# Kernel optimization log

Hardware: AMD Instinct MI355X
Metric: run time of the kernel (lower is better)

Reference implementation:

```python
import jax, jax.numpy as jnp
import numpy as np

B, S, D = 16, 1024, 1024
H, HD = 16, 64  # head_dim = D // H
INIT_STD = 0.002
DEFAULT_BETA = 1.0 / np.sqrt(HD)


def setup_inputs() -> dict:
    key = jax.random.key(0)
    k1, k2, k3 = jax.random.split(key, 3)
    x = jax.random.normal(k1, (B, S, D), dtype=jnp.float32)
    q_proj_weight = jax.random.normal(k2, (H, HD, D), dtype=jnp.float32) * INIT_STD
    k_proj_weight = jax.random.normal(k3, (H, HD, D), dtype=jnp.float32) * INIT_STD
    beta = jnp.full((H,), DEFAULT_BETA, dtype=jnp.float32)
    return {"x": x, "q_proj_weight": q_proj_weight, "k_proj_weight": k_proj_weight, "beta": beta}


def reference(x, q_proj_weight, k_proj_weight, beta):
    # q, k: (B, S, H, HD)
    q = jnp.einsum('bse,hde->bshd', x, q_proj_weight)
    k = jnp.einsum('bse,hde->bshd', x, k_proj_weight)
    # scores: (B, H, S_query, S_key) with per-head beta temperature
    scores = jnp.einsum('bshd,bthd,h->bhst', q, k, beta)
    # self-attention exclusion: mask the diagonal (B == C) with -inf
    seq = scores.shape[-1]
    diag = jnp.eye(seq, dtype=bool)
    scores = jnp.where(diag[None, None], -jnp.inf, scores)
    # stable logsumexp over keys, then energy = -sum_h,s lse / beta_h
    lse = jax.nn.logsumexp(scores, axis=-1)  # (B, H, S)
    energy = -(lse / beta[None, :, None]).sum()
    return energy
```

## Files before the change

### kernel.cpp

```cpp
#include <hip/hip_runtime.h>
#include <hip/hip_bf16.h>


using short8  = __attribute__((ext_vector_type(8))) short;
using f32x4   = __attribute__((ext_vector_type(4))) float;
using ushort8 = __attribute__((ext_vector_type(8))) unsigned short;
using float4v = __attribute__((ext_vector_type(4))) float;

#define B_  16
#define S_  1024
#define D_  1024
#define H_  16
#define HD_ 64

__device__ inline unsigned short f2bf(float f) {
  union { float f; unsigned u; } v; v.f = f;
  unsigned r = v.u + 0x7FFFu + ((v.u >> 16) & 1u);
  return (unsigned short)(r >> 16);
}

__global__ __launch_bounds__(256) void cvt_bf16_k(const float* __restrict__ in,
                                                  unsigned short* __restrict__ out, int n8) {
  int i = blockIdx.x * 256 + threadIdx.x;
  if (i >= n8) return;
  const float4v* p = (const float4v*)in;
  float4v a = p[2 * i], b = p[2 * i + 1];
  ushort8 r;
  r[0] = f2bf(a[0]); r[1] = f2bf(a[1]); r[2] = f2bf(a[2]); r[3] = f2bf(a[3]);
  r[4] = f2bf(b[0]); r[5] = f2bf(b[1]); r[6] = f2bf(b[2]); r[7] = f2bf(b[3]);
  ((ushort8*)out)[i] = r;
}

__global__ void zero_out_k(float* o) { if (threadIdx.x == 0) *o = 0.f; }

__device__ inline void gload_lds16(const void* g, void* l) {
  __builtin_amdgcn_global_load_lds((const __attribute__((address_space(1))) void*)g,
                                   (__attribute__((address_space(3))) void*)l, 16, 0, 0);
}

__device__ inline void stage_tile(const char* src, int stride, char* lds, int tid) {
  int lane = tid & 63, wave = tid >> 6;
#pragma unroll
  for (int r = 0; r < 4; ++r) {
    int o   = r * 4096 + wave * 1024 + lane * 16;
    int row = o >> 7;
    int kb  = o & 127;
    int skb = kb ^ ((row & 7) << 4);
    gload_lds16(src + (size_t)row * stride + skb, lds + (r * 4096 + wave * 1024));
  }
}

__device__ inline short8 ld_frag(const char* lds, int row, int kk, int lane) {
  int kb   = kk * 64 + ((lane >> 4) << 4);
  int addr = row * 128 + (kb ^ ((row & 7) << 4));
  return *(const short8*)(lds + addr);
}

__global__ __launch_bounds__(256) void proj_gemm_k(const unsigned short* __restrict__ Xb,
                                                   const unsigned short* __restrict__ Wqb,
                                                   const unsigned short* __restrict__ Wkb,
                                                   unsigned short* __restrict__ Qg,
                                                   unsigned short* __restrict__ Kg) {
  __shared__ char As[16384];
  __shared__ char Bs[16384];
  const int tid = threadIdx.x, lane = tid & 63, wave = tid >> 6;
  const int wr = wave >> 1, wc = wave & 1;
  const int m0 = blockIdx.x * 128, n0 = blockIdx.y * 128;
  const unsigned short* W = blockIdx.z ? Wkb : Wqb;
  unsigned short* Out = blockIdx.z ? Kg : Qg;
  const char* Abase = (const char*)Xb + (size_t)m0 * (D_ * 2);
  const char* Bbase = (const char*)W  + (size_t)n0 * (D_ * 2);

  f32x4 acc[4][4];
#pragma unroll
  for (int i = 0; i < 4; ++i)
#pragma unroll
    for (int j = 0; j < 4; ++j)
#pragma unroll
      for (int q = 0; q < 4; ++q) acc[i][j][q] = 0.f;

  for (int kt = 0; kt < D_ / 64; ++kt) {
    stage_tile(Abase + kt * 128, D_ * 2, As, tid);
    stage_tile(Bbase + kt * 128, D_ * 2, Bs, tid);
    __syncthreads();
#pragma unroll
    for (int kk = 0; kk < 2; ++kk) {
      short8 a[4], b[4];
#pragma unroll
      for (int i = 0; i < 4; ++i) a[i] = ld_frag(As, wr * 64 + i * 16 + (lane & 15), kk, lane);
#pragma unroll
      for (int i = 0; i < 4; ++i) b[i] = ld_frag(Bs, wc * 64 + i * 16 + (lane & 15), kk, lane);
#pragma unroll
      for (int i = 0; i < 4; ++i)
#pragma unroll
        for (int j = 0; j < 4; ++j)
          acc[i][j] = __builtin_amdgcn_mfma_f32_16x16x32_bf16(a[i], b[j], acc[i][j], 0, 0, 0);
    }
    __syncthreads();
  }

#pragma unroll
  for (int mi = 0; mi < 4; ++mi)
#pragma unroll
    for (int ni = 0; ni < 4; ++ni)
#pragma unroll
      for (int j = 0; j < 4; ++j) {
        int m = m0 + wr * 64 + mi * 16 + ((lane >> 4) << 2) + j;
        int n = n0 + wc * 64 + ni * 16 + (lane & 15);
        int bb = m >> 10, s = m & (S_ - 1);
        int h = n >> 6, hd = n & (HD_ - 1);
        Out[(((size_t)bb * H_ + h) * S_ + s) * HD_ + hd] = f2bf(acc[mi][ni][j]);
      }
}

__global__ __launch_bounds__(256) void attn_lse_k(const unsigned short* __restrict__ Qg,
                                                  const unsigned short* __restrict__ Kg,
                                                  const float* __restrict__ beta,
                                                  float* __restrict__ out) {
  __shared__ char Qs[16384];
  __shared__ char Ks[16384];
  __shared__ float wsum[4];
  const int tid = threadIdx.x, lane = tid & 63, wave = tid >> 6;
  const int qt = blockIdx.x, h = blockIdx.y, b = blockIdx.z;
  const int q0 = qt * 128;
  const char* qbase = (const char*)Qg + (((size_t)b * H_ + h) * S_) * (HD_ * 2);
  const char* kbase = (const char*)Kg + (((size_t)b * H_ + h) * S_) * (HD_ * 2);

  stage_tile(qbase + (size_t)q0 * 128, 128, Qs, tid);
  const float bet = beta[h];

  float l_run[2][4];
#pragma unroll
  for (int mi = 0; mi < 2; ++mi)
#pragma unroll
    for (int j = 0; j < 4; ++j) l_run[mi][j] = 0.f;

  for (int kt = 0; kt < 8; ++kt) {
    stage_tile(kbase + (size_t)kt * 128 * 128, 128, Ks, tid);
    __syncthreads();

    f32x4 acc[2][8];
#pragma unroll
    for (int i = 0; i < 2; ++i)
#pragma unroll
      for (int j = 0; j < 8; ++j)
#pragma unroll
        for (int q = 0; q < 4; ++q) acc[i][j][q] = 0.f;

#pragma unroll
    for (int kk = 0; kk < 2; ++kk) {
      short8 a[2], kb[8];
#pragma unroll
      for (int mi = 0; mi < 2; ++mi)
        a[mi] = ld_frag(Qs, wave * 32 + mi * 16 + (lane & 15), kk, lane);
#pragma unroll
      for (int ni = 0; ni < 8; ++ni)
        kb[ni] = ld_frag(Ks, ni * 16 + (lane & 15), kk, lane);
#pragma unroll
      for (int mi = 0; mi < 2; ++mi)
#pragma unroll
        for (int ni = 0; ni < 8; ++ni)
          acc[mi][ni] = __builtin_amdgcn_mfma_f32_16x16x32_bf16(a[mi], kb[ni], acc[mi][ni], 0, 0, 0);
    }

    const bool dg = (kt == qt);
    float rs[2][4];
#pragma unroll
    for (int mi = 0; mi < 2; ++mi)
#pragma unroll
      for (int j = 0; j < 4; ++j) rs[mi][j] = 0.f;

#pragma unroll
    for (int mi = 0; mi < 2; ++mi)
#pragma unroll
      for (int ni = 0; ni < 8; ++ni) {
        f32x4 v = acc[mi][ni];
#pragma unroll
        for (int j = 0; j < 4; ++j) {
          float s = v[j] * bet;
          if (dg && (wave * 32 + mi * 16 + ((lane >> 4) << 2) + j) == (ni * 16 + (lane & 15)))
            s = -1e30f;
          rs[mi][j] += __expf(s);
        }
      }

#pragma unroll
    for (int mi = 0; mi < 2; ++mi)
#pragma unroll
      for (int j = 0; j < 4; ++j) {
        float v = rs[mi][j];
        v += __shfl_xor(v, 1); v += __shfl_xor(v, 2);
        v += __shfl_xor(v, 4); v += __shfl_xor(v, 8);
        l_run[mi][j] += v;
      }
    __syncthreads();
  }

  float local = 0.f;
#pragma unroll
  for (int mi = 0; mi < 2; ++mi)
#pragma unroll
    for (int j = 0; j < 4; ++j) local += __logf(l_run[mi][j]);
  local += __shfl_xor(local, 16);
  local += __shfl_xor(local, 32);
  if (lane == 0) wsum[wave] = local;
  __syncthreads();
  if (tid == 0) {
    float t = wsum[0] + wsum[1] + wsum[2] + wsum[3];
    atomicAdd(out, -t / bet);
  }
}

extern "C" void kernel_launch(void* const* d_in, const int* in_sizes, int n_in,
                              void* d_out, int out_size, void* d_ws, size_t ws_size,
                              hipStream_t stream) {
  const float* x    = (const float*)d_in[0];
  const float* qw   = (const float*)d_in[1];
  const float* kw   = (const float*)d_in[2];
  const float* beta = (const float*)d_in[3];
  float* out = (float*)d_out;

  char* ws = (char*)d_ws;
  unsigned short* Xb  = (unsigned short*)(ws);
  unsigned short* Wqb = (unsigned short*)(ws + 33554432);
  unsigned short* Wkb = (unsigned short*)(ws + 35651584);
  unsigned short* Qg  = (unsigned short*)(ws + 37748736);
  unsigned short* Kg  = (unsigned short*)(ws + 71303168);

  cvt_bf16_k<<<8192, 256, 0, stream>>>(x,  Xb,  (B_ * S_ * D_) / 8);
  cvt_bf16_k<<<512,  256, 0, stream>>>(qw, Wqb, (H_ * HD_ * D_) / 8);
  cvt_bf16_k<<<512,  256, 0, stream>>>(kw, Wkb, (H_ * HD_ * D_) / 8);
  zero_out_k<<<1, 64, 0, stream>>>(out);
  proj_gemm_k<<<dim3(128, 8, 2), 256, 0, stream>>>(Xb, Wqb, Wkb, Qg, Kg);
  attn_lse_k<<<dim3(8, H_, B_), 256, 0, stream>>>(Qg, Kg, beta, out);
}
```

Measured before the change: 272.1 us.

## Fold beta*log2e into Q projection, double-buffer K tiles, remap workgroups per XCD

The projection GEMM now scales Q by beta*log2(e) at store time, so the attention kernel can use exp2/log2 directly without a per-element multiply. The attention kernel keeps Q fragments in registers, double-buffers K tiles in LDS so the next tile loads while the current one computes, and splits the diagonal-mask path out of the common loop. It also defers the row-sum shuffles to the end and raises wave priority around the MFMAs. Both kernels use a flat grid with a workgroup index remap that groups neighbouring tiles onto the same XCD for cache locality. Rounding Q to bf16 after scaling shifts numerics slightly.

```diff
diff --git a/kernel.cpp b/kernel.cpp
--- a/kernel.cpp
+++ b/kernel.cpp
@@ -12,6 +12,19 @@
 #define D_  1024
 #define H_  16
 #define HD_ 64
+#define LOG2E 1.4426950408889634f
+#define LN2   0.6931471805599453f
+
+#if __has_builtin(__builtin_amdgcn_exp2f)
+#define EXP2F(x) __builtin_amdgcn_exp2f(x)
+#else
+#define EXP2F(x) exp2f(x)
+#endif
+#if __has_builtin(__builtin_amdgcn_logf)
+#define LOG2F(x) __builtin_amdgcn_logf(x)
+#else
+#define LOG2F(x) log2f(x)
+#endif
 
 __device__ inline unsigned short f2bf(float f) {
   union { float f; unsigned u; } v; v.f = f;
@@ -59,15 +72,18 @@
 __global__ __launch_bounds__(256) void proj_gemm_k(const unsigned short* __restrict__ Xb,
                                                    const unsigned short* __restrict__ Wqb,
                                                    const unsigned short* __restrict__ Wkb,
+                                                   const float* __restrict__ beta,
                                                    unsigned short* __restrict__ Qg,
                                                    unsigned short* __restrict__ Kg) {
   __shared__ char As[16384];
   __shared__ char Bs[16384];
   const int tid = threadIdx.x, lane = tid & 63, wave = tid >> 6;
   const int wr = wave >> 1, wc = wave & 1;
-  const int m0 = blockIdx.x * 128, n0 = blockIdx.y * 128;
-  const unsigned short* W = blockIdx.z ? Wkb : Wqb;
-  unsigned short* Out = blockIdx.z ? Kg : Qg;
+  const int wgid = (blockIdx.x & 7) * 256 + (blockIdx.x >> 3);
+  const int mt = wgid >> 4, nz = wgid & 15;
+  const int m0 = mt * 128, n0 = (nz & 7) * 128, z = nz >> 3;
+  const unsigned short* W = z ? Wkb : Wqb;
+  unsigned short* Out = z ? Kg : Qg;
   const char* Abase = (const char*)Xb + (size_t)m0 * (D_ * 2);
   const char* Bbase = (const char*)W  + (size_t)n0 * (D_ * 2);
 
@@ -99,6 +115,7 @@
     __syncthreads();
   }
 
+  const float scl = z ? 1.0f : beta[(n0 >> 6) + wc] * LOG2E;
 #pragma unroll
   for (int mi = 0; mi < 4; ++mi)
 #pragma unroll
@@ -109,7 +126,7 @@
         int n = n0 + wc * 64 + ni * 16 + (lane & 15);
         int bb = m >> 10, s = m & (S_ - 1);
         int h = n >> 6, hd = n & (HD_ - 1);
-        Out[(((size_t)bb * H_ + h) * S_ + s) * HD_ + hd] = f2bf(acc[mi][ni][j]);
+        Out[(((size_t)bb * H_ + h) * S_ + s) * HD_ + hd] = f2bf(acc[mi][ni][j] * scl);
       }
 }
 
@@ -117,97 +134,100 @@
                                                   const unsigned short* __restrict__ Kg,
                                                   const float* __restrict__ beta,
                                                   float* __restrict__ out) {
-  __shared__ char Qs[16384];
-  __shared__ char Ks[16384];
+  __shared__ char Ks[2][16384];
   __shared__ float wsum[4];
   const int tid = threadIdx.x, lane = tid & 63, wave = tid >> 6;
-  const int qt = blockIdx.x, h = blockIdx.y, b = blockIdx.z;
-  const int q0 = qt * 128;
+  const int wgid = (blockIdx.x & 7) * 256 + (blockIdx.x >> 3);
+  const int qt = wgid & 7, hb = wgid >> 3;
+  const int h = hb & 15, b = hb >> 4;
   const char* qbase = (const char*)Qg + (((size_t)b * H_ + h) * S_) * (HD_ * 2);
   const char* kbase = (const char*)Kg + (((size_t)b * H_ + h) * S_) * (HD_ * 2);
 
-  stage_tile(qbase + (size_t)q0 * 128, 128, Qs, tid);
-  const float bet = beta[h];
-
-  float l_run[2][4];
+  stage_tile(qbase + (size_t)qt * 16384, 128, Ks[0], tid);
+  __syncthreads();
+  short8 qa[2][2];
 #pragma unroll
   for (int mi = 0; mi < 2; ++mi)
 #pragma unroll
-    for (int j = 0; j < 4; ++j) l_run[mi][j] = 0.f;
-
+    for (int kk = 0; kk < 2; ++kk)
+      qa[mi][kk] = ld_frag(Ks[0], wave * 32 + mi * 16 + (lane & 15), kk, lane);
+  stage_tile(kbase, 128, Ks[1], tid);
+  __syncthreads();
+
+  float rs[2][4];
+#pragma unroll
+  for (int mi = 0; mi < 2; ++mi)
+#pragma unroll
+    for (int j = 0; j < 4; ++j) rs[mi][j] = 0.f;
+
+  int cur = 1;
   for (int kt = 0; kt < 8; ++kt) {
-    stage_tile(kbase + (size_t)kt * 128 * 128, 128, Ks, tid);
+    if (kt < 7) stage_tile(kbase + (size_t)(kt + 1) * 16384, 128, Ks[cur ^ 1], tid);
+
+    f32x4 acc[2][8];
+#pragma unroll
+    for (int i = 0; i < 2; ++i)
+#pragma unroll
+      for (int j = 0; j < 8; ++j)
+#pragma unroll
+        for (int q = 0; q < 4; ++q) acc[i][j][q] = 0.f;
+
+    __builtin_amdgcn_s_setprio(1);
+#pragma unroll
+    for (int kk = 0; kk < 2; ++kk)
+#pragma unroll
+      for (int ni = 0; ni < 8; ++ni) {
+        short8 kf = ld_frag(Ks[cur], ni * 16 + (lane & 15), kk, lane);
+        acc[0][ni] = __builtin_amdgcn_mfma_f32_16x16x32_bf16(qa[0][kk], kf, acc[0][ni], 0, 0, 0);
+        acc[1][ni] = __builtin_amdgcn_mfma_f32_16x16x32_bf16(qa[1][kk], kf, acc[1][ni], 0, 0, 0);
+      }
+    __builtin_amdgcn_s_setprio(0);
+
+    if (kt == qt) {
+#pragma unroll
+      for (int mi = 0; mi < 2; ++mi)
+#pragma unroll
+        for (int ni = 0; ni < 8; ++ni) {
+          f32x4 v = acc[mi][ni];
+#pragma unroll
+          for (int j = 0; j < 4; ++j) {
+            int row = wave * 32 + mi * 16 + ((lane >> 4) << 2) + j;
+            int col = ni * 16 + (lane & 15);
+            float s = (row == col) ? -1e30f : v[j];
+            rs[mi][j] += EXP2F(s);
+          }
+        }
+    } else {
+#pragma unroll
+      for (int mi = 0; mi < 2; ++mi)
+#pragma unroll
+        for (int ni = 0; ni < 8; ++ni) {
+          f32x4 v = acc[mi][ni];
+#pragma unroll
+          for (int j = 0; j < 4; ++j) rs[mi][j] += EXP2F(v[j]);
+        }
+    }
     __syncthreads();
-
-    f32x4 acc[2][8];
-#pragma unroll
-    for (int i = 0; i < 2; ++i)
-#pragma unroll
-      for (int j = 0; j < 8; ++j)
-#pragma unroll
-        for (int q = 0; q < 4; ++q) acc[i][j][q] = 0.f;
-
-#pragma unroll
-    for (int kk = 0; kk < 2; ++kk) {
-      short8 a[2], kb[8];
-#pragma unroll
-      for (int mi = 0; mi < 2; ++mi)
-        a[mi] = ld_frag(Qs, wave * 32 + mi * 16 + (lane & 15), kk, lane);
-#pragma unroll
-      for (int ni = 0; ni < 8; ++ni)
-        kb[ni] = ld_frag(Ks, ni * 16 + (lane & 15), kk, lane);
-#pragma unroll
-      for (int mi = 0; mi < 2; ++mi)
-#pragma unroll
-        for (int ni = 0; ni < 8; ++ni)
-          acc[mi][ni] = __builtin_amdgcn_mfma_f32_16x16x32_bf16(a[mi], kb[ni], acc[mi][ni], 0, 0, 0);
+    cur ^= 1;
+  }
+
+  float local = 0.f;
+#pragma unroll
+  for (int mi = 0; mi < 2; ++mi)
+#pragma unroll
+    for (int j = 0; j < 4; ++j) {
+      float v = rs[mi][j];
+      v += __shfl_xor(v, 1); v += __shfl_xor(v, 2);
+      v += __shfl_xor(v, 4); v += __shfl_xor(v, 8);
+      local += LOG2F(v);
     }
-
-    const bool dg = (kt == qt);
-    float rs[2][4];
-#pragma unroll
-    for (int mi = 0; mi < 2; ++mi)
-#pragma unroll
-      for (int j = 0; j < 4; ++j) rs[mi][j] = 0.f;
-
-#pragma unroll
-    for (int mi = 0; mi < 2; ++mi)
-#pragma unroll
-      for (int ni = 0; ni < 8; ++ni) {
-        f32x4 v = acc[mi][ni];
-#pragma unroll
-        for (int j = 0; j < 4; ++j) {
-          float s = v[j] * bet;
-          if (dg && (wave * 32 + mi * 16 + ((lane >> 4) << 2) + j) == (ni * 16 + (lane & 15)))
-            s = -1e30f;
-          rs[mi][j] += __expf(s);
-        }
-      }
-
-#pragma unroll
-    for (int mi = 0; mi < 2; ++mi)
-#pragma unroll
-      for (int j = 0; j < 4; ++j) {
-        float v = rs[mi][j];
-        v += __shfl_xor(v, 1); v += __shfl_xor(v, 2);
-        v += __shfl_xor(v, 4); v += __shfl_xor(v, 8);
-        l_run[mi][j] += v;
-      }
-    __syncthreads();
-  }
-
-  float local = 0.f;
-#pragma unroll
-  for (int mi = 0; mi < 2; ++mi)
-#pragma unroll
-    for (int j = 0; j < 4; ++j) local += __logf(l_run[mi][j]);
   local += __shfl_xor(local, 16);
   local += __shfl_xor(local, 32);
   if (lane == 0) wsum[wave] = local;
   __syncthreads();
   if (tid == 0) {
     float t = wsum[0] + wsum[1] + wsum[2] + wsum[3];
-    atomicAdd(out, -t / bet);
+    atomicAdd(out, -t * LN2 / beta[h]);
   }
 }
 
@@ -231,6 +251,6 @@
   cvt_bf16_k<<<512,  256, 0, stream>>>(qw, Wqb, (H_ * HD_ * D_) / 8);
   cvt_bf16_k<<<512,  256, 0, stream>>>(kw, Wkb, (H_ * HD_ * D_) / 8);
   zero_out_k<<<1, 64, 0, stream>>>(out);
-  proj_gemm_k<<<dim3(128, 8, 2), 256, 0, stream>>>(Xb, Wqb, Wkb, Qg, Kg);
-  attn_lse_k<<<dim3(8, H_, B_), 256, 0, stream>>>(Qg, Kg, beta, out);
-}
+  proj_gemm_k<<<2048, 256, 0, stream>>>(Xb, Wqb, Wkb, beta, Qg, Kg);
+  attn_lse_k<<<2048, 256, 0, stream>>>(Qg, Kg, beta, out);
+}
```

After: 253.8 us. -6.7%, faster.
